# Kernel tuning notes

Hardware: AMD Instinct MI355X
Metric: run time of the kernel (lower is better)

## Reference

```python
import jax, jax.numpy as jnp
import numpy as np

RATIO = 0.5  # init arg of CAGPool_layer
B, N_PER_GRAPH, D, DEG = 256, 512, 256, 32


def setup_inputs() -> dict:
    key = jax.random.key(0)
    k1, k2, k3, k4 = jax.random.split(key, 4)
    N = B * N_PER_GRAPH
    Eg = N_PER_GRAPH * DEG  # edges per graph
    x = jax.random.normal(k1, (N, D), dtype=jnp.float32)
    # within-graph random edges, then offset to global node ids
    src = jax.random.randint(k2, (B, Eg), 0, N_PER_GRAPH, dtype=jnp.int32)
    dst = jax.random.randint(k3, (B, Eg), 0, N_PER_GRAPH, dtype=jnp.int32)
    off = (jnp.arange(B, dtype=jnp.int32) * N_PER_GRAPH)[:, None]
    edge_index = jnp.stack([(src + off).reshape(-1), (dst + off).reshape(-1)], axis=0)
    batch = jnp.repeat(jnp.arange(B, dtype=jnp.int32), N_PER_GRAPH)
    pool_vector = jax.random.normal(k4, (B, D), dtype=jnp.float32)
    c_size = jnp.full((B,), N_PER_GRAPH, dtype=jnp.int32)  # uniform graph sizes
    return {"x": x, "edge_index": edge_index, "batch": batch,
            "pool_vector": pool_vector, "c_size": c_size}


def reference(x, edge_index, batch, pool_vector, c_size):
    N, d = x.shape
    Bn = pool_vector.shape[0]
    n = N // Bn  # uniform nodes per graph (c_size is constant = n)
    k = int(np.ceil(RATIO * n))

    # x_ = pool_vector repeated c_size[i] times == gather by batch (uniform sizes)
    x_ = pool_vector[batch]                                   # [N, d]
    score = jnp.sum(x * x_, axis=1) / jnp.linalg.norm(x_, axis=1)  # [N]

    # per-graph top-k (dense [B, n] view; graphs are contiguous blocks of n nodes)
    _, idx = jax.lax.top_k(score.reshape(Bn, n), k)           # [B, k] local ids
    perm = (idx + (jnp.arange(Bn, dtype=idx.dtype) * n)[:, None]).reshape(-1)  # [B*k]

    # gather kept nodes, sigmoid-gate by their scores
    x_out = x[perm] * jax.nn.sigmoid(score[perm])[:, None]    # [B*k, d]
    batch_out = batch[perm]                                   # [B*k]

    # filter_adj: remap node ids, mask edges with a dropped endpoint.
    # (torch version compacts the edge list; we keep static shape [2, E] and
    #  mark dropped edges with -1 plus a boolean validity mask.)
    nodemap = jnp.full((N,), -1, dtype=jnp.int32).at[perm].set(
        jnp.arange(perm.shape[0], dtype=jnp.int32))
    row = nodemap[edge_index[0]]
    col = nodemap[edge_index[1]]
    valid = (row >= 0) & (col >= 0)
    edge_index_new = jnp.stack([jnp.where(valid, row, -1),
                                jnp.where(valid, col, -1)], axis=0)
    return x_out, edge_index_new, batch_out, perm, valid
```

## Files before the change

kernel.cpp:

```cpp
#include <hip/hip_runtime.h>
#include <math.h>


__global__ __launch_bounds__(1024)
void score_rank_kernel(const float4* __restrict__ x4,
                       const float4* __restrict__ pool4,
                       int* __restrict__ nodemap,
                       int* __restrict__ perm_int,
                       float* __restrict__ gate,
                       float* __restrict__ out,
                       long off_batch, long off_perm,
                       int n, int k) {
    extern __shared__ double s[];
    int b = blockIdx.x;
    int t = threadIdx.x;
    int w = t >> 6, l = t & 63;
    int nw = blockDim.x >> 6;

    float4 pv = pool4[(size_t)b * 64 + l];
    double px = pv.x, py = pv.y, pz = pv.z, pw = pv.w;
    double nn = px * px + py * py + pz * pz + pw * pw;
    for (int off = 32; off > 0; off >>= 1) nn += __shfl_xor(nn, off, 64);
    double inv = 1.0 / sqrt(nn);

    int npw = n / nw;
    const float4* xg = x4 + ((size_t)b * n + (size_t)w * npw) * 64;
    for (int i = 0; i < npw; i += 4) {
        const float4* xa = xg + (size_t)i * 64;
        float4 va = xa[l], vb = xa[64 + l], vc = xa[128 + l], vd = xa[192 + l];
        double da = (double)va.x * px + (double)va.y * py
                  + (double)va.z * pz + (double)va.w * pw;
        double db = (double)vb.x * px + (double)vb.y * py
                  + (double)vb.z * pz + (double)vb.w * pw;
        double dc = (double)vc.x * px + (double)vc.y * py
                  + (double)vc.z * pz + (double)vc.w * pw;
        double dd = (double)vd.x * px + (double)vd.y * py
                  + (double)vd.z * pz + (double)vd.w * pw;
        for (int off = 32; off > 0; off >>= 1) {
            da += __shfl_xor(da, off, 64);
            db += __shfl_xor(db, off, 64);
            dc += __shfl_xor(dc, off, 64);
            dd += __shfl_xor(dd, off, 64);
        }
        if (l == 0) {
            int base = w * npw + i;
            s[base]     = da * inv;
            s[base + 1] = db * inv;
            s[base + 2] = dc * inv;
            s[base + 3] = dd * inv;
        }
    }
    __syncthreads();

    if (t < n) {
        double st = s[t];
        int rank = 0;
#pragma unroll 8
        for (int j = 0; j < n; ++j) {
            double sj = s[j];
            rank += (int)((sj > st) || (sj == st && j < t));
        }
        int gid = b * n + t;
        if (rank < k) {
            int p = b * k + rank;
            nodemap[gid] = p;
            perm_int[p] = gid;
            gate[p] = (float)(1.0 / (1.0 + exp(-st)));
            out[off_batch + p] = (float)b;
            out[off_perm + p]  = (float)gid;
        } else {
            nodemap[gid] = -1;
        }
    }
}

__global__ void out_kernel(const float4* __restrict__ x4,
                           const float* __restrict__ gate,
                           const int* __restrict__ perm_int,
                           const int4* __restrict__ ei_src,
                           const int4* __restrict__ ei_dst,
                           const int* __restrict__ nodemap,
                           float4* __restrict__ out0,
                           float4* __restrict__ out_row,
                           float4* __restrict__ out_col,
                           float4* __restrict__ out_valid,
                           int nv, int GA, long epg4, int n) {
    extern __shared__ int smem[];
    int bid = blockIdx.x;
    if (bid < GA) {
        int w = threadIdx.x >> 6, l = threadIdx.x & 63;
        int p = bid * 4 + w;
        int gid = perm_int[p];
        float g = gate[p];
        const float4* xr = x4 + (size_t)gid * nv;
        float4* orow = out0 + (size_t)p * nv;
        for (int j = l; j < nv; j += 64) {
            float4 v = xr[j];
            v.x *= g; v.y *= g; v.z *= g; v.w *= g;
            orow[j] = v;
        }
    } else {
        long blk = bid - GA;
        long e4base = blk * 512;
        long g = e4base / epg4;
        int base = (int)(g * (long)n);
        for (int i = threadIdx.x; i < n; i += 256)
            smem[i] = nodemap[base + i];
        __syncthreads();
#pragma unroll
        for (int half = 0; half < 2; ++half) {
            long e = e4base + half * 256 + threadIdx.x;
            int4 sv = ei_src[e];
            int4 dv = ei_dst[e];
            int r0 = smem[sv.x - base], r1 = smem[sv.y - base];
            int r2 = smem[sv.z - base], r3 = smem[sv.w - base];
            int c0 = smem[dv.x - base], c1 = smem[dv.y - base];
            int c2 = smem[dv.z - base], c3 = smem[dv.w - base];
            bool v0 = (r0 >= 0) & (c0 >= 0);
            bool v1 = (r1 >= 0) & (c1 >= 0);
            bool v2 = (r2 >= 0) & (c2 >= 0);
            bool v3 = (r3 >= 0) & (c3 >= 0);
            float4 rv = { v0 ? (float)r0 : -1.0f, v1 ? (float)r1 : -1.0f,
                          v2 ? (float)r2 : -1.0f, v3 ? (float)r3 : -1.0f };
            float4 cv = { v0 ? (float)c0 : -1.0f, v1 ? (float)c1 : -1.0f,
                          v2 ? (float)c2 : -1.0f, v3 ? (float)c3 : -1.0f };
            float4 vv = { v0 ? 1.0f : 0.0f, v1 ? 1.0f : 0.0f,
                          v2 ? 1.0f : 0.0f, v3 ? 1.0f : 0.0f };
            out_row[e]   = rv;
            out_col[e]   = cv;
            out_valid[e] = vv;
        }
    }
}

__global__ void norm_kernel(const float* __restrict__ pool,
                            double* __restrict__ inv_norm, int D) {
    int b = blockIdx.x;
    int l = threadIdx.x;
    double acc = 0.0;
    for (int j = l; j < D; j += 64) {
        double v = (double)pool[(size_t)b * D + j];
        acc += v * v;
    }
    for (int off = 32; off > 0; off >>= 1) acc += __shfl_down(acc, off, 64);
    if (l == 0) inv_norm[b] = 1.0 / sqrt(acc);
}

__global__ void score_kernel(const float* __restrict__ x,
                             const float* __restrict__ pool,
                             const double* __restrict__ inv_norm,
                             double* __restrict__ scores,
                             int D, int n) {
    int node = blockIdx.x * 4 + (threadIdx.x >> 6);
    int l = threadIdx.x & 63;
    int b = node / n;
    const float* xr = x + (size_t)node * D;
    const float* pr = pool + (size_t)b * D;
    double acc = 0.0;
    for (int j = l; j < D; j += 64)
        acc += (double)xr[j] * (double)pr[j];
    for (int off = 32; off > 0; off >>= 1) acc += __shfl_down(acc, off, 64);
    if (l == 0) scores[node] = acc * inv_norm[b];
}

__global__ void rank_kernel(const double* __restrict__ scores,
                            int* __restrict__ nodemap,
                            int* __restrict__ perm_int,
                            float* __restrict__ out,
                            long off_batch, long off_perm,
                            int n, int k) {
    extern __shared__ double s[];
    int b = blockIdx.x;
    int t = threadIdx.x;
    int gid = b * n + t;
    double st = scores[gid];
    s[t] = st;
    __syncthreads();
    int rank = 0;
    for (int j = 0; j < n; ++j) {
        double sj = s[j];
        rank += (int)((sj > st) || (sj == st && j < t));
    }
    if (rank < k) {
        int p = b * k + rank;
        nodemap[gid] = p;
        perm_int[p] = gid;
        out[off_batch + p] = (float)b;
        out[off_perm + p]  = (float)gid;
    } else {
        nodemap[gid] = -1;
    }
}

__global__ void gather_kernel(const float* __restrict__ x,
                              const double* __restrict__ scores,
                              const int* __restrict__ perm_int,
                              float* __restrict__ out0, int D) {
    int p = blockIdx.x;
    int l = threadIdx.x;
    int gid = perm_int[p];
    double sc = scores[gid];
    float g = (float)(1.0 / (1.0 + exp(-sc)));
    const float* xr = x + (size_t)gid * D;
    float* orow = out0 + (size_t)p * D;
    for (int j = l; j < D; j += 64) orow[j] = xr[j] * g;
}

__global__ void edge_kernel(const int* __restrict__ ei,
                            const int* __restrict__ nodemap,
                            float* __restrict__ out,
                            long off_e, long off_valid, long E) {
    long e = (long)blockIdx.x * blockDim.x + threadIdx.x;
    if (e >= E) return;
    int r = nodemap[ei[e]];
    int c = nodemap[ei[E + e]];
    bool valid = (r >= 0) && (c >= 0);
    out[off_e + e]     = valid ? (float)r : -1.0f;
    out[off_e + E + e] = valid ? (float)c : -1.0f;
    out[off_valid + e] = valid ? 1.0f : 0.0f;
}

extern "C" void kernel_launch(void* const* d_in, const int* in_sizes, int n_in,
                              void* d_out, int out_size, void* d_ws, size_t ws_size,
                              hipStream_t stream) {
    const float* x    = (const float*)d_in[0];
    const int*   ei   = (const int*)d_in[1];
    const float* pool = (const float*)d_in[3];

    const int B = in_sizes[4];
    const int D = in_sizes[3] / B;
    const long N = (long)in_sizes[0] / D;
    const long E = (long)in_sizes[1] / 2;
    const int n = (int)(N / B);
    const int k = (n + 1) / 2;
    const long Eg = E / B;

    char* ws = (char*)d_ws;
    double* scores   = (double*)ws;                         ws += (size_t)N * 8;
    double* inv_norm = (double*)ws;                         ws += (size_t)B * 8;
    int*    nodemap  = (int*)ws;                            ws += (size_t)N * 4;
    int*    perm_int = (int*)ws;                            ws += (size_t)B * ((N/B+1)/2) * 4;
    float*  gate     = (float*)ws;

    float* out = (float*)d_out;
    const long o0 = 0;
    const long o1 = o0 + (long)B * k * D;
    const long o2 = o1 + 2 * E;
    const long o3 = o2 + (long)B * k;
    const long o4 = o3 + (long)B * k;

    bool fused_sr_ok = (D == 256) && (n % 64 == 0) && (n <= 1024);
    bool fused_out_ok = fused_sr_ok && ((long)B * k % 4 == 0) &&
                        (E % 2048 == 0) && (Eg % 2048 == 0) &&
                        (o1 % 4 == 0) && ((o1 + E) % 4 == 0) && (o4 % 4 == 0);

    if (fused_out_ok) {
        score_rank_kernel<<<B, 1024, (size_t)n * sizeof(double), stream>>>(
            (const float4*)x, (const float4*)pool,
            nodemap, perm_int, gate, out, o2, o3, n, k);
        int GA = (int)((long)B * k / 4);
        int GB = (int)(E / 2048);
        out_kernel<<<GA + GB, 256, (size_t)n * sizeof(int), stream>>>(
            (const float4*)x, gate, perm_int,
            (const int4*)ei, (const int4*)(ei + E), nodemap,
            (float4*)(out + o0), (float4*)(out + o1),
            (float4*)(out + o1 + E), (float4*)(out + o4),
            D / 4, GA, Eg / 4, n);
    } else {
        norm_kernel<<<B, 64, 0, stream>>>(pool, inv_norm, D);
        score_kernel<<<(int)(N / 4), 256, 0, stream>>>(
            x, pool, inv_norm, scores, D, n);
        rank_kernel<<<B, n, (size_t)n * sizeof(double), stream>>>(
            scores, nodemap, perm_int, out, o2, o3, n, k);
        gather_kernel<<<(int)((long)B * k), 64, 0, stream>>>(
            x, scores, perm_int, out + o0, D);
        edge_kernel<<<(int)((E + 255) / 256), 256, 0, stream>>>(
            ei, nodemap, out, o1, o4, E);
    }
}
```

Baseline: 84.27 us.

## Fuse scoring, ranking, gather and edge remap into one per-graph kernel

Merges the score/rank kernel and the gather/edge kernel into a single kernel with one block per graph. The node map, permutation and gates stay in shared memory instead of going through global memory. It also software-prefetches the next x rows during the scoring loop. This removes a launch and global intermediate traffic, but all work now runs on only B blocks, which may reduce memory-level parallelism for the large edge and gather writes.

```diff
diff --git a/kernel.cpp b/kernel.cpp
--- a/kernel.cpp
+++ b/kernel.cpp
@@ -3,19 +3,26 @@
 
 
 __global__ __launch_bounds__(1024)
-void score_rank_kernel(const float4* __restrict__ x4,
-                       const float4* __restrict__ pool4,
-                       int* __restrict__ nodemap,
-                       int* __restrict__ perm_int,
-                       float* __restrict__ gate,
-                       float* __restrict__ out,
-                       long off_batch, long off_perm,
-                       int n, int k) {
-    extern __shared__ double s[];
-    int b = blockIdx.x;
-    int t = threadIdx.x;
-    int w = t >> 6, l = t & 63;
-    int nw = blockDim.x >> 6;
+void mega_kernel(const float4* __restrict__ x4,
+                 const float4* __restrict__ pool4,
+                 const int4* __restrict__ ei_src4,
+                 const int4* __restrict__ ei_dst4,
+                 float4* __restrict__ out0,
+                 float4* __restrict__ out_row,
+                 float4* __restrict__ out_col,
+                 float4* __restrict__ out_valid,
+                 float* __restrict__ out_batch,
+                 float* __restrict__ out_perm,
+                 int n, int k, int Eg4) {
+    __shared__ double s[1024];
+    __shared__ int    nmap[1024];
+    __shared__ int    perm_l[512];
+    __shared__ float  gate_l[512];
+
+    const int b = blockIdx.x;
+    const int t = threadIdx.x;
+    const int w = t >> 6, l = t & 63;
+    const int nw = blockDim.x >> 6;
 
     float4 pv = pool4[(size_t)b * 64 + l];
     double px = pv.x, py = pv.y, pz = pv.z, pw = pv.w;
@@ -23,11 +30,17 @@
     for (int off = 32; off > 0; off >>= 1) nn += __shfl_xor(nn, off, 64);
     double inv = 1.0 / sqrt(nn);
 
-    int npw = n / nw;
+    const int npw = n / nw;
     const float4* xg = x4 + ((size_t)b * n + (size_t)w * npw) * 64;
+
+    float4 va = xg[l], vb = xg[64 + l], vc = xg[128 + l], vd = xg[192 + l];
     for (int i = 0; i < npw; i += 4) {
-        const float4* xa = xg + (size_t)i * 64;
-        float4 va = xa[l], vb = xa[64 + l], vc = xa[128 + l], vd = xa[192 + l];
+        float4 na, nb, nc, nd;
+        bool more = (i + 4 < npw);
+        if (more) {
+            const float4* xn = xg + (size_t)(i + 4) * 64;
+            na = xn[l]; nb = xn[64 + l]; nc = xn[128 + l]; nd = xn[192 + l];
+        }
         double da = (double)va.x * px + (double)va.y * py
                   + (double)va.z * pz + (double)va.w * pw;
         double db = (double)vb.x * px + (double)vb.y * py
@@ -49,6 +62,7 @@
             s[base + 2] = dc * inv;
             s[base + 3] = dd * inv;
         }
+        if (more) { va = na; vb = nb; vc = nc; vd = nd; }
     }
     __syncthreads();
 
@@ -60,62 +74,43 @@
             double sj = s[j];
             rank += (int)((sj > st) || (sj == st && j < t));
         }
-        int gid = b * n + t;
         if (rank < k) {
             int p = b * k + rank;
-            nodemap[gid] = p;
-            perm_int[p] = gid;
-            gate[p] = (float)(1.0 / (1.0 + exp(-st)));
-            out[off_batch + p] = (float)b;
-            out[off_perm + p]  = (float)gid;
+            nmap[t] = p;
+            perm_l[rank] = t;
+            gate_l[rank] = (float)(1.0 / (1.0 + exp(-st)));
+            out_batch[p] = (float)b;
+            out_perm[p]  = (float)(b * n + t);
         } else {
-            nodemap[gid] = -1;
-        }
-    }
-}
-
-__global__ void out_kernel(const float4* __restrict__ x4,
-                           const float* __restrict__ gate,
-                           const int* __restrict__ perm_int,
-                           const int4* __restrict__ ei_src,
-                           const int4* __restrict__ ei_dst,
-                           const int* __restrict__ nodemap,
-                           float4* __restrict__ out0,
-                           float4* __restrict__ out_row,
-                           float4* __restrict__ out_col,
-                           float4* __restrict__ out_valid,
-                           int nv, int GA, long epg4, int n) {
-    extern __shared__ int smem[];
-    int bid = blockIdx.x;
-    if (bid < GA) {
-        int w = threadIdx.x >> 6, l = threadIdx.x & 63;
-        int p = bid * 4 + w;
-        int gid = perm_int[p];
-        float g = gate[p];
-        const float4* xr = x4 + (size_t)gid * nv;
-        float4* orow = out0 + (size_t)p * nv;
-        for (int j = l; j < nv; j += 64) {
-            float4 v = xr[j];
+            nmap[t] = -1;
+        }
+    }
+    __syncthreads();
+
+    {
+        const int total = k << 6;
+        const size_t xbase = (size_t)b * n * 64;
+        const size_t obase = (size_t)b * k * 64;
+        for (int c = t; c < total; c += 1024) {
+            int row = c >> 6, col = c & 63;
+            int gl = perm_l[row];
+            float g = gate_l[row];
+            float4 v = x4[xbase + (size_t)gl * 64 + col];
             v.x *= g; v.y *= g; v.z *= g; v.w *= g;
-            orow[j] = v;
-        }
-    } else {
-        long blk = bid - GA;
-        long e4base = blk * 512;
-        long g = e4base / epg4;
-        int base = (int)(g * (long)n);
-        for (int i = threadIdx.x; i < n; i += 256)
-            smem[i] = nodemap[base + i];
-        __syncthreads();
-#pragma unroll
-        for (int half = 0; half < 2; ++half) {
-            long e = e4base + half * 256 + threadIdx.x;
-            int4 sv = ei_src[e];
-            int4 dv = ei_dst[e];
-            int r0 = smem[sv.x - base], r1 = smem[sv.y - base];
-            int r2 = smem[sv.z - base], r3 = smem[sv.w - base];
-            int c0 = smem[dv.x - base], c1 = smem[dv.y - base];
-            int c2 = smem[dv.z - base], c3 = smem[dv.w - base];
+            out0[obase + (size_t)row * 64 + col] = v;
+        }
+    }
+
+    {
+        const int base_e4 = b * Eg4;
+        const int nbase = b * n;
+        for (int i = t; i < Eg4; i += 1024) {
+            int4 sv = ei_src4[base_e4 + i];
+            int4 dv = ei_dst4[base_e4 + i];
+            int r0 = nmap[sv.x - nbase], r1 = nmap[sv.y - nbase];
+            int r2 = nmap[sv.z - nbase], r3 = nmap[sv.w - nbase];
+            int c0 = nmap[dv.x - nbase], c1 = nmap[dv.y - nbase];
+            int c2 = nmap[dv.z - nbase], c3 = nmap[dv.w - nbase];
             bool v0 = (r0 >= 0) & (c0 >= 0);
             bool v1 = (r1 >= 0) & (c1 >= 0);
             bool v2 = (r2 >= 0) & (c2 >= 0);
@@ -126,9 +121,9 @@
                           v2 ? (float)c2 : -1.0f, v3 ? (float)c3 : -1.0f };
             float4 vv = { v0 ? 1.0f : 0.0f, v1 ? 1.0f : 0.0f,
                           v2 ? 1.0f : 0.0f, v3 ? 1.0f : 0.0f };
-            out_row[e]   = rv;
-            out_col[e]   = cv;
-            out_valid[e] = vv;
+            out_row[base_e4 + i]   = rv;
+            out_col[base_e4 + i]   = cv;
+            out_valid[base_e4 + i] = vv;
         }
     }
 }
@@ -169,16 +164,16 @@
                             float* __restrict__ out,
                             long off_batch, long off_perm,
                             int n, int k) {
-    extern __shared__ double s[];
+    extern __shared__ double sdyn[];
     int b = blockIdx.x;
     int t = threadIdx.x;
     int gid = b * n + t;
     double st = scores[gid];
-    s[t] = st;
+    sdyn[t] = st;
     __syncthreads();
     int rank = 0;
     for (int j = 0; j < n; ++j) {
-        double sj = s[j];
+        double sj = sdyn[j];
         rank += (int)((sj > st) || (sj == st && j < t));
     }
     if (rank < k) {
@@ -235,13 +230,6 @@
     const int k = (n + 1) / 2;
     const long Eg = E / B;
 
-    char* ws = (char*)d_ws;
-    double* scores   = (double*)ws;                         ws += (size_t)N * 8;
-    double* inv_norm = (double*)ws;                         ws += (size_t)B * 8;
-    int*    nodemap  = (int*)ws;                            ws += (size_t)N * 4;
-    int*    perm_int = (int*)ws;                            ws += (size_t)B * ((N/B+1)/2) * 4;
-    float*  gate     = (float*)ws;
-
     float* out = (float*)d_out;
     const long o0 = 0;
     const long o1 = o0 + (long)B * k * D;
@@ -249,24 +237,25 @@
     const long o3 = o2 + (long)B * k;
     const long o4 = o3 + (long)B * k;
 
-    bool fused_sr_ok = (D == 256) && (n % 64 == 0) && (n <= 1024);
-    bool fused_out_ok = fused_sr_ok && ((long)B * k % 4 == 0) &&
-                        (E % 2048 == 0) && (Eg % 2048 == 0) &&
-                        (o1 % 4 == 0) && ((o1 + E) % 4 == 0) && (o4 % 4 == 0);
-
-    if (fused_out_ok) {
-        score_rank_kernel<<<B, 1024, (size_t)n * sizeof(double), stream>>>(
+    bool mega_ok = (D == 256) && (n % 64 == 0) && (n <= 1024) &&
+                   (Eg % 4 == 0) && (E % 4 == 0) &&
+                   (o1 % 4 == 0) && ((o1 + E) % 4 == 0) && (o4 % 4 == 0);
+
+    if (mega_ok) {
+        mega_kernel<<<B, 1024, 0, stream>>>(
             (const float4*)x, (const float4*)pool,
-            nodemap, perm_int, gate, out, o2, o3, n, k);
-        int GA = (int)((long)B * k / 4);
-        int GB = (int)(E / 2048);
-        out_kernel<<<GA + GB, 256, (size_t)n * sizeof(int), stream>>>(
-            (const float4*)x, gate, perm_int,
-            (const int4*)ei, (const int4*)(ei + E), nodemap,
+            (const int4*)ei, (const int4*)(ei + E),
             (float4*)(out + o0), (float4*)(out + o1),
             (float4*)(out + o1 + E), (float4*)(out + o4),
-            D / 4, GA, Eg / 4, n);
+            out + o2, out + o3,
+            n, k, (int)(Eg / 4));
     } else {
+        char* ws = (char*)d_ws;
+        double* scores   = (double*)ws;                 ws += (size_t)N * 8;
+        double* inv_norm = (double*)ws;                 ws += (size_t)B * 8;
+        int*    nodemap  = (int*)ws;                    ws += (size_t)N * 4;
+        int*    perm_int = (int*)ws;
+
         norm_kernel<<<B, 64, 0, stream>>>(pool, inv_norm, D);
         score_kernel<<<(int)(N / 4), 256, 0, stream>>>(
             x, pool, inv_norm, scores, D, n);
```

Result: slower. 88.17 us (+4.6%).

## Split fused score-rank kernel into wide score pass and separate rank kernel

Applied to the files above, without the earlier changes.

Replaces the single per-graph score+rank kernel (256 blocks of 1024 threads, each wave looping over many rows) with a score kernel launched over N/16 blocks of 256 threads, each wave computing four row dot products in fp64 and writing them to a workspace buffer. A separate rank kernel then loads scores into shared memory and does the O(n^2) rank count plus the gate/output writes. This exposes far more blocks for the bandwidth-bound x read, at the cost of an extra launch and a round trip of scores through global memory.

```diff
diff --git a/kernel.cpp b/kernel.cpp
--- a/kernel.cpp
+++ b/kernel.cpp
@@ -2,20 +2,13 @@
 #include <math.h>
 
 
-__global__ __launch_bounds__(1024)
-void score_rank_kernel(const float4* __restrict__ x4,
-                       const float4* __restrict__ pool4,
-                       int* __restrict__ nodemap,
-                       int* __restrict__ perm_int,
-                       float* __restrict__ gate,
-                       float* __restrict__ out,
-                       long off_batch, long off_perm,
-                       int n, int k) {
-    extern __shared__ double s[];
-    int b = blockIdx.x;
-    int t = threadIdx.x;
-    int w = t >> 6, l = t & 63;
-    int nw = blockDim.x >> 6;
+__global__ __launch_bounds__(256)
+void score_hi_kernel(const float4* __restrict__ x4,
+                     const float4* __restrict__ pool4,
+                     double* __restrict__ scores, int n) {
+    const int w = threadIdx.x >> 6, l = threadIdx.x & 63;
+    const int row = blockIdx.x * 16 + w * 4;
+    const int b = row / n;
 
     float4 pv = pool4[(size_t)b * 64 + l];
     double px = pv.x, py = pv.y, pz = pv.z, pw = pv.w;
@@ -23,54 +16,59 @@
     for (int off = 32; off > 0; off >>= 1) nn += __shfl_xor(nn, off, 64);
     double inv = 1.0 / sqrt(nn);
 
-    int npw = n / nw;
-    const float4* xg = x4 + ((size_t)b * n + (size_t)w * npw) * 64;
-    for (int i = 0; i < npw; i += 4) {
-        const float4* xa = xg + (size_t)i * 64;
-        float4 va = xa[l], vb = xa[64 + l], vc = xa[128 + l], vd = xa[192 + l];
-        double da = (double)va.x * px + (double)va.y * py
-                  + (double)va.z * pz + (double)va.w * pw;
-        double db = (double)vb.x * px + (double)vb.y * py
-                  + (double)vb.z * pz + (double)vb.w * pw;
-        double dc = (double)vc.x * px + (double)vc.y * py
-                  + (double)vc.z * pz + (double)vc.w * pw;
-        double dd = (double)vd.x * px + (double)vd.y * py
-                  + (double)vd.z * pz + (double)vd.w * pw;
-        for (int off = 32; off > 0; off >>= 1) {
-            da += __shfl_xor(da, off, 64);
-            db += __shfl_xor(db, off, 64);
-            dc += __shfl_xor(dc, off, 64);
-            dd += __shfl_xor(dd, off, 64);
-        }
-        if (l == 0) {
-            int base = w * npw + i;
-            s[base]     = da * inv;
-            s[base + 1] = db * inv;
-            s[base + 2] = dc * inv;
-            s[base + 3] = dd * inv;
-        }
-    }
+    const float4* xa = x4 + (size_t)row * 64;
+    float4 va = xa[l], vb = xa[64 + l], vc = xa[128 + l], vd = xa[192 + l];
+    double da = (double)va.x * px + (double)va.y * py
+              + (double)va.z * pz + (double)va.w * pw;
+    double db = (double)vb.x * px + (double)vb.y * py
+              + (double)vb.z * pz + (double)vb.w * pw;
+    double dc = (double)vc.x * px + (double)vc.y * py
+              + (double)vc.z * pz + (double)vc.w * pw;
+    double dd = (double)vd.x * px + (double)vd.y * py
+              + (double)vd.z * pz + (double)vd.w * pw;
+    for (int off = 32; off > 0; off >>= 1) {
+        da += __shfl_xor(da, off, 64);
+        db += __shfl_xor(db, off, 64);
+        dc += __shfl_xor(dc, off, 64);
+        dd += __shfl_xor(dd, off, 64);
+    }
+    if (l == 0) {
+        scores[row]     = da * inv;
+        scores[row + 1] = db * inv;
+        scores[row + 2] = dc * inv;
+        scores[row + 3] = dd * inv;
+    }
+}
+
+__global__ void rank_gate_kernel(const double* __restrict__ scores,
+                                 int* __restrict__ nodemap,
+                                 int* __restrict__ perm_int,
+                                 float* __restrict__ gate,
+                                 float* __restrict__ out,
+                                 long off_batch, long off_perm,
+                                 int n, int k) {
+    extern __shared__ double s[];
+    int b = blockIdx.x;
+    int t = threadIdx.x;
+    int gid = b * n + t;
+    double st = scores[gid];
+    s[t] = st;
     __syncthreads();
-
-    if (t < n) {
-        double st = s[t];
-        int rank = 0;
+    int rank = 0;
 #pragma unroll 8
-        for (int j = 0; j < n; ++j) {
-            double sj = s[j];
-            rank += (int)((sj > st) || (sj == st && j < t));
-        }
-        int gid = b * n + t;
-        if (rank < k) {
-            int p = b * k + rank;
-            nodemap[gid] = p;
-            perm_int[p] = gid;
-            gate[p] = (float)(1.0 / (1.0 + exp(-st)));
-            out[off_batch + p] = (float)b;
-            out[off_perm + p]  = (float)gid;
-        } else {
-            nodemap[gid] = -1;
-        }
+    for (int j = 0; j < n; ++j) {
+        double sj = s[j];
+        rank += (int)((sj > st) || (sj == st && j < t));
+    }
+    if (rank < k) {
+        int p = b * k + rank;
+        nodemap[gid] = p;
+        perm_int[p] = gid;
+        gate[p] = (float)(1.0 / (1.0 + exp(-st)));
+        out[off_batch + p] = (float)b;
+        out[off_perm + p]  = (float)gid;
+    } else {
+        nodemap[gid] = -1;
     }
 }
 
@@ -169,16 +167,16 @@
                             float* __restrict__ out,
                             long off_batch, long off_perm,
                             int n, int k) {
-    extern __shared__ double s[];
+    extern __shared__ double sdyn[];
     int b = blockIdx.x;
     int t = threadIdx.x;
     int gid = b * n + t;
     double st = scores[gid];
-    s[t] = st;
+    sdyn[t] = st;
     __syncthreads();
     int rank = 0;
     for (int j = 0; j < n; ++j) {
-        double sj = s[j];
+        double sj = sdyn[j];
         rank += (int)((sj > st) || (sj == st && j < t));
     }
     if (rank < k) {
@@ -236,10 +234,10 @@
     const long Eg = E / B;
 
     char* ws = (char*)d_ws;
-    double* scores   = (double*)ws;                         ws += (size_t)N * 8;
-    double* inv_norm = (double*)ws;                         ws += (size_t)B * 8;
-    int*    nodemap  = (int*)ws;                            ws += (size_t)N * 4;
-    int*    perm_int = (int*)ws;                            ws += (size_t)B * ((N/B+1)/2) * 4;
+    double* scores   = (double*)ws;                 ws += (size_t)N * 8;
+    double* inv_norm = (double*)ws;                 ws += (size_t)B * 8;
+    int*    nodemap  = (int*)ws;                    ws += (size_t)N * 4;
+    int*    perm_int = (int*)ws;                    ws += (size_t)B * ((size_t)(n + 1) / 2) * 4;
     float*  gate     = (float*)ws;
 
     float* out = (float*)d_out;
@@ -249,15 +247,16 @@
     const long o3 = o2 + (long)B * k;
     const long o4 = o3 + (long)B * k;
 
-    bool fused_sr_ok = (D == 256) && (n % 64 == 0) && (n <= 1024);
-    bool fused_out_ok = fused_sr_ok && ((long)B * k % 4 == 0) &&
-                        (E % 2048 == 0) && (Eg % 2048 == 0) &&
-                        (o1 % 4 == 0) && ((o1 + E) % 4 == 0) && (o4 % 4 == 0);
-
-    if (fused_out_ok) {
-        score_rank_kernel<<<B, 1024, (size_t)n * sizeof(double), stream>>>(
-            (const float4*)x, (const float4*)pool,
-            nodemap, perm_int, gate, out, o2, o3, n, k);
+    bool fast_ok = (D == 256) && (n % 16 == 0) && (n <= 1024) &&
+                   ((long)B * k % 4 == 0) &&
+                   (E % 2048 == 0) && (Eg % 2048 == 0) &&
+                   (o1 % 4 == 0) && ((o1 + E) % 4 == 0) && (o4 % 4 == 0);
+
+    if (fast_ok) {
+        score_hi_kernel<<<(int)(N / 16), 256, 0, stream>>>(
+            (const float4*)x, (const float4*)pool, scores, n);
+        rank_gate_kernel<<<B, n, (size_t)n * sizeof(double), stream>>>(
+            scores, nodemap, perm_int, gate, out, o2, o3, n, k);
         int GA = (int)((long)B * k / 4);
         int GB = (int)(E / 2048);
         out_kernel<<<GA + GB, 256, (size_t)n * sizeof(int), stream>>>(
```

After: 82.70 us. No clear change (-1.9%).
